# Optimization experiments

Hardware: AMD Instinct MI355X
Metric: run time of the kernel (lower is better)

The kernel has to match this reference:

```python
import jax, jax.numpy as jnp
import numpy as np

B, T, C, H = 4, 2048, 1024, 16
D = C // H  # head_dim = 64


def setup_inputs() -> dict:
    key = jax.random.key(0)
    k1, k2, k3 = jax.random.split(key, 3)
    x = jax.random.normal(k1, (B, T, C), dtype=jnp.float32)
    # nn.Linear weights: [out_features, in_features]
    W_attn = jax.random.normal(k2, (3 * C, C), dtype=jnp.float32) * (1.0 / np.sqrt(C))
    W_proj = jax.random.normal(k3, (C, C), dtype=jnp.float32) * (1.0 / np.sqrt(C))
    b_proj = jnp.zeros((C,), dtype=jnp.float32)
    return {"x": x, "W_attn": W_attn, "W_proj": W_proj, "b_proj": b_proj}


def reference(x, W_attn, W_proj, b_proj):
    Bx, Tx, Cx = x.shape
    # fused QKV projection (no bias), then split
    qkv = jnp.einsum('btc,oc->bto', x, W_attn)            # [B,T,3C]
    q, k, v = jnp.split(qkv, 3, axis=-1)                  # each [B,T,C]
    # [B,T,C] -> [B,H,T,D]
    def heads(t):
        return t.reshape(Bx, Tx, H, D).transpose(0, 2, 1, 3)
    q, k, v = heads(q), heads(k), heads(v)
    scale = 1.0 / np.sqrt(D).astype(np.float32)
    att = jnp.einsum('bhqd,bhkd->bhqk', q, k) * scale     # [B,H,T,T], no causal mask
    att = jax.nn.softmax(att, axis=-1)
    y = jnp.einsum('bhqk,bhkd->bhqd', att, v)             # [B,H,T,D]
    y = y.transpose(0, 2, 1, 3).reshape(Bx, Tx, Cx)       # [B,T,C]
    out = jnp.einsum('btc,oc->bto', y, W_proj) + b_proj   # output projection
    return out
```

## Files before the change

kernel.cpp:

```cpp
#include <hip/hip_runtime.h>


typedef _Float16 f16x8 __attribute__((ext_vector_type(8)));
typedef _Float16 f16x4 __attribute__((ext_vector_type(4)));
typedef _Float16 f16x2 __attribute__((ext_vector_type(2)));
typedef float f32x4 __attribute__((ext_vector_type(4)));

__device__ __forceinline__ void gl_lds16(const _Float16* g, _Float16* l) {
  __builtin_amdgcn_global_load_lds(
      (const __attribute__((address_space(1))) void*)g,
      (__attribute__((address_space(3))) void*)l, 16, 0, 0);
}

__device__ __forceinline__ float fexp2(float x) {
#if __has_builtin(__builtin_amdgcn_exp2f)
  return __builtin_amdgcn_exp2f(x);
#else
  return exp2f(x);
#endif
}

__global__ __launch_bounds__(256) void cvt_f32_f16(const float* __restrict__ src,
                                                   _Float16* __restrict__ dst, int n) {
  int i = (blockIdx.x * 256 + threadIdx.x) * 8;
  int stride = gridDim.x * 256 * 8;
  for (; i < n; i += stride) {
    float4 a = *(const float4*)(src + i);
    float4 b = *(const float4*)(src + i + 4);
    f16x8 o = {(_Float16)a.x, (_Float16)a.y, (_Float16)a.z, (_Float16)a.w,
               (_Float16)b.x, (_Float16)b.y, (_Float16)b.z, (_Float16)b.w};
    *(f16x8*)(dst + i) = o;
  }
}

template <bool BIAS, bool OUT_F16>
__global__ __launch_bounds__(256)
void gemm_bt(const _Float16* __restrict__ A, const _Float16* __restrict__ B,
             void* __restrict__ C, const float* __restrict__ bias,
             int M, int N, int K) {
  __shared__ _Float16 sA[128 * 64];
  __shared__ _Float16 sB[128 * 64];
  const int tid = threadIdx.x;
  const int w = tid >> 6, l = tid & 63, l15 = l & 15, l4 = l >> 4;
  const int wm = w >> 1, wn = w & 1;
  const size_t m0 = (size_t)blockIdx.y * 128, n0 = (size_t)blockIdx.x * 128;

  f32x4 acc[4][4] = {};

  const int sr = tid >> 3;
  const int sc8 = (tid & 7) ^ ((tid >> 3) & 7);
  const _Float16* aSrc = A + (m0 + sr) * (size_t)K + sc8 * 8;
  const _Float16* bSrc = B + (n0 + sr) * (size_t)K + sc8 * 8;
  _Float16* aDst = sA + tid * 8;
  _Float16* bDst = sB + tid * 8;
  const size_t K32 = 32 * (size_t)K;

  const int e7 = l15 & 7;

  for (int k0 = 0; k0 < K; k0 += 64) {
    __syncthreads();
#pragma unroll
    for (int j = 0; j < 4; ++j) {
      gl_lds16(aSrc + j * K32 + k0, aDst + j * 2048);
      gl_lds16(bSrc + j * K32 + k0, bDst + j * 2048);
    }
    __syncthreads();
#pragma unroll
    for (int ks = 0; ks < 2; ++ks) {
      const int cs_ = ((ks * 4 + l4) ^ e7) * 8;
      f16x8 af[4], bf[4];
#pragma unroll
      for (int i = 0; i < 4; ++i) {
        af[i] = *(const f16x8*)(sA + (wm * 64 + i * 16 + l15) * 64 + cs_);
        bf[i] = *(const f16x8*)(sB + (wn * 64 + i * 16 + l15) * 64 + cs_);
      }
#pragma unroll
      for (int i = 0; i < 4; ++i)
#pragma unroll
        for (int j = 0; j < 4; ++j)
          acc[i][j] = __builtin_amdgcn_mfma_f32_16x16x32_f16(af[i], bf[j], acc[i][j], 0, 0, 0);
    }
  }

#pragma unroll
  for (int i = 0; i < 4; ++i)
#pragma unroll
    for (int j = 0; j < 4; ++j) {
      size_t row = m0 + wm * 64 + i * 16 + l4 * 4;
      size_t col = n0 + wn * 64 + j * 16 + l15;
      float bv = 0.0f;
      if (BIAS) bv = bias[col];
#pragma unroll
      for (int rr = 0; rr < 4; ++rr) {
        float v = acc[i][j][rr] + bv;
        if (OUT_F16)
          ((_Float16*)C)[(row + rr) * N + col] = (_Float16)v;
        else
          ((float*)C)[(row + rr) * N + col] = v;
      }
    }
}

__global__ __launch_bounds__(256, 4)
void attn_kernel(const _Float16* __restrict__ qkv, _Float16* __restrict__ y16) {
  const int lin = blockIdx.x;
  const int xcd = lin & 7;
  const int bh = xcd * 8 + (lin >> 7);
  const int qt = (lin >> 3) & 15;
  const int b = bh >> 4, h = bh & 15;
  const int tid = threadIdx.x;
  const int w = tid >> 6, l = tid & 63, l15 = l & 15, l4 = l >> 4;

  __shared__ _Float16 sK[128 * 64];
  __shared__ _Float16 sVt[64][136];

  const size_t rowbase = (size_t)b * 2048;
  const int qcol = h * 64, kcol = 1024 + h * 64, vcol = 2048 + h * 64;

  f16x8 bq[2][2];
  {
    const _Float16 csf = (_Float16)(0.125f * 1.44269504f);
#pragma unroll
    for (int qs = 0; qs < 2; ++qs) {
      size_t qrow = rowbase + qt * 128 + w * 32 + qs * 16 + l15;
#pragma unroll
      for (int ks = 0; ks < 2; ++ks) {
        f16x8 v = *(const f16x8*)(qkv + qrow * 3072 + qcol + ks * 32 + l4 * 8);
#pragma unroll
        for (int e = 0; e < 8; ++e) v[e] *= csf;
        bq[qs][ks] = v;
      }
    }
  }

  f32x4 accy[2][4] = {};
  f32x4 accl[2] = {};

  const _Float16 one0 = (l15 == 0) ? (_Float16)1.0f : (_Float16)0.0f;
  const f16x4 bv1 = {one0, one0, one0, one0};

  const int krow = w * 8 + (l >> 3);
  const int csrc = (l & 7) ^ (l >> 3);
  const _Float16* kSrc0 = qkv + (rowbase + krow) * 3072 + kcol + csrc * 8;
  _Float16* kDst0 = sK + w * 8 * 64 + l * 8;

  const int vrow = 2 * l, vd0 = w * 16;
  const _Float16* vSrc0 = qkv + (rowbase + vrow) * 3072 + vcol + vd0;

  f16x8 va0 = *(const f16x8*)(vSrc0);
  f16x8 va1 = *(const f16x8*)(vSrc0 + 8);
  f16x8 vb0 = *(const f16x8*)(vSrc0 + 3072);
  f16x8 vb1 = *(const f16x8*)(vSrc0 + 3072 + 8);

  for (int kb = 0; kb < 16; ++kb) {
    __syncthreads();
    {
      const _Float16* ks_ = kSrc0 + (size_t)kb * 128 * 3072;
#pragma unroll
      for (int j = 0; j < 4; ++j) gl_lds16(ks_ + (size_t)j * 32 * 3072, kDst0 + j * 2048);
#pragma unroll
      for (int e = 0; e < 8; ++e) {
        f16x2 p0; p0[0] = va0[e]; p0[1] = vb0[e];
        *(f16x2*)(&sVt[vd0 + e][vrow]) = p0;
        f16x2 p1; p1[0] = va1[e]; p1[1] = vb1[e];
        *(f16x2*)(&sVt[vd0 + 8 + e][vrow]) = p1;
      }
    }
    __syncthreads();

    if (kb + 1 < 16) {
      const _Float16* vs_ = vSrc0 + (size_t)(kb + 1) * 128 * 3072;
      va0 = *(const f16x8*)(vs_);
      va1 = *(const f16x8*)(vs_ + 8);
      vb0 = *(const f16x8*)(vs_ + 3072);
      vb1 = *(const f16x8*)(vs_ + 3072 + 8);
    }

#pragma unroll
    for (int sub = 0; sub < 2; ++sub) {
      f32x4 st[2][4] = {};
      __builtin_amdgcn_s_setprio(1);
#pragma unroll
      for (int m = 0; m < 4; ++m) {
        const int row = sub * 64 + m * 16 + l15;
#pragma unroll
        for (int ks = 0; ks < 2; ++ks) {
          const int cs_ = (ks * 4 + l4) ^ (l15 & 7);
          f16x8 ak = *(const f16x8*)(sK + row * 64 + cs_ * 8);
          st[0][m] = __builtin_amdgcn_mfma_f32_16x16x32_f16(ak, bq[0][ks], st[0][m], 0, 0, 0);
          st[1][m] = __builtin_amdgcn_mfma_f32_16x16x32_f16(ak, bq[1][ks], st[1][m], 0, 0, 0);
        }
      }
      __builtin_amdgcn_s_setprio(0);

      f16x4 pa[2][4];
#pragma unroll
      for (int qs = 0; qs < 2; ++qs) {
#pragma unroll
        for (int m = 0; m < 4; ++m) {
          float p0 = fexp2(st[qs][m][0]);
          float p1 = fexp2(st[qs][m][1]);
          float p2 = fexp2(st[qs][m][2]);
          float p3 = fexp2(st[qs][m][3]);
#if __has_builtin(__builtin_amdgcn_cvt_pkrtz)
          auto lo = __builtin_amdgcn_cvt_pkrtz(p0, p1);
          auto hi = __builtin_amdgcn_cvt_pkrtz(p2, p3);
          f16x4 pv;
          pv[0] = lo[0]; pv[1] = lo[1]; pv[2] = hi[0]; pv[3] = hi[1];
          pa[qs][m] = pv;
#else
          f16x4 pv;
          pv[0] = (_Float16)p0; pv[1] = (_Float16)p1;
          pv[2] = (_Float16)p2; pv[3] = (_Float16)p3;
          pa[qs][m] = pv;
#endif
        }
      }

      __builtin_amdgcn_s_setprio(1);
#pragma unroll
      for (int m = 0; m < 4; ++m) {
        const int kc = sub * 64 + m * 16 + l4 * 4;
        accl[0] = __builtin_amdgcn_mfma_f32_16x16x16f16(bv1, pa[0][m], accl[0], 0, 0, 0);
        accl[1] = __builtin_amdgcn_mfma_f32_16x16x16f16(bv1, pa[1][m], accl[1], 0, 0, 0);
#pragma unroll
        for (int dt = 0; dt < 4; ++dt) {
          f16x4 bv = *(const f16x4*)(&sVt[dt * 16 + l15][kc]);
          accy[0][dt] = __builtin_amdgcn_mfma_f32_16x16x16f16(bv, pa[0][m], accy[0][dt], 0, 0, 0);
          accy[1][dt] = __builtin_amdgcn_mfma_f32_16x16x16f16(bv, pa[1][m], accy[1][dt], 0, 0, 0);
        }
      }
      __builtin_amdgcn_s_setprio(0);
    }
  }

#pragma unroll
  for (int qs = 0; qs < 2; ++qs) {
    const float lsum = __shfl(accl[qs][0], l15);
    const float rinv = 1.0f / lsum;
    const size_t row = rowbase + qt * 128 + w * 32 + qs * 16 + l15;
#pragma unroll
    for (int dt = 0; dt < 4; ++dt) {
      f16x4 ov;
#pragma unroll
      for (int r = 0; r < 4; ++r) ov[r] = (_Float16)(accy[qs][dt][r] * rinv);
      *(f16x4*)(y16 + row * 1024 + h * 64 + dt * 16 + l4 * 4) = ov;
    }
  }
}

extern "C" void kernel_launch(void* const* d_in, const int* in_sizes, int n_in,
                              void* d_out, int out_size, void* d_ws, size_t ws_size,
                              hipStream_t stream) {
  (void)in_sizes; (void)n_in; (void)out_size; (void)ws_size;
  const float* x  = (const float*)d_in[0];
  const float* Wa = (const float*)d_in[1];
  const float* Wp = (const float*)d_in[2];
  const float* bp = (const float*)d_in[3];
  float* out = (float*)d_out;

  char* ws = (char*)d_ws;
  _Float16* x16   = (_Float16*)ws; ws += (size_t)8192 * 1024 * 2;
  _Float16* Wa16  = (_Float16*)ws; ws += (size_t)3072 * 1024 * 2;
  _Float16* Wp16  = (_Float16*)ws; ws += (size_t)1024 * 1024 * 2;
  _Float16* qkv16 = (_Float16*)ws; ws += (size_t)8192 * 3072 * 2;
  _Float16* y16   = (_Float16*)ws; ws += (size_t)8192 * 1024 * 2;

  cvt_f32_f16<<<4096, 256, 0, stream>>>(x, x16, 8192 * 1024);
  cvt_f32_f16<<<1536, 256, 0, stream>>>(Wa, Wa16, 3072 * 1024);
  cvt_f32_f16<<<512, 256, 0, stream>>>(Wp, Wp16, 1024 * 1024);

  gemm_bt<false, true><<<dim3(24, 64), 256, 0, stream>>>(x16, Wa16, (void*)qkv16, nullptr,
                                                         8192, 3072, 1024);
  attn_kernel<<<1024, 256, 0, stream>>>(qkv16, y16);
  gemm_bt<true, false><<<dim3(8, 64), 256, 0, stream>>>(y16, Wp16, (void*)out, bp,
                                                        8192, 1024, 1024);
}
```

Measured before the change: 285.7 us.

## Use 16x16x32 MFMA for PV product via permuted K row loading

Switches the P·V and row-sum MFMAs from 16x16x16 to 16x16x32 instructions, concatenating two score tiles into an 8-wide f16 operand. For the K dimension of the 32-wide MFMA to line up with the S tile layout, K rows are loaded into shared memory in a permuted order (pkey), so score columns match V rows. This halves the number of PV MFMA issues and widens the LDS reads of V, at the cost of a subtle index permutation that must stay consistent.

```diff
diff --git a/kernel.cpp b/kernel.cpp
--- a/kernel.cpp
+++ b/kernel.cpp
@@ -137,11 +137,12 @@
   f32x4 accl[2] = {};
 
   const _Float16 one0 = (l15 == 0) ? (_Float16)1.0f : (_Float16)0.0f;
-  const f16x4 bv1 = {one0, one0, one0, one0};
-
-  const int krow = w * 8 + (l >> 3);
+  const f16x8 ones8 = {one0, one0, one0, one0, one0, one0, one0, one0};
+
+  const int rho = w * 8 + (l >> 3);
+  const int pkey = (rho & 3) | ((rho & 0x10) >> 2) | ((rho & 0xC) << 1);
   const int csrc = (l & 7) ^ (l >> 3);
-  const _Float16* kSrc0 = qkv + (rowbase + krow) * 3072 + kcol + csrc * 8;
+  const _Float16* kSrc0 = qkv + (rowbase + pkey) * 3072 + kcol + csrc * 8;
   _Float16* kDst0 = sK + w * 8 * 64 + l * 8;
 
   const int vrow = 2 * l, vd0 = w * 16;
@@ -193,41 +194,47 @@
       }
       __builtin_amdgcn_s_setprio(0);
 
-      f16x4 pa[2][4];
+      f16x8 pa8[2][2];
 #pragma unroll
       for (int qs = 0; qs < 2; ++qs) {
 #pragma unroll
-        for (int m = 0; m < 4; ++m) {
-          float p0 = fexp2(st[qs][m][0]);
-          float p1 = fexp2(st[qs][m][1]);
-          float p2 = fexp2(st[qs][m][2]);
-          float p3 = fexp2(st[qs][m][3]);
+        for (int c = 0; c < 2; ++c) {
+          f16x4 half_[2];
+#pragma unroll
+          for (int mm = 0; mm < 2; ++mm) {
+            const int m = 2 * c + mm;
+            float p0 = fexp2(st[qs][m][0]);
+            float p1 = fexp2(st[qs][m][1]);
+            float p2 = fexp2(st[qs][m][2]);
+            float p3 = fexp2(st[qs][m][3]);
 #if __has_builtin(__builtin_amdgcn_cvt_pkrtz)
-          auto lo = __builtin_amdgcn_cvt_pkrtz(p0, p1);
-          auto hi = __builtin_amdgcn_cvt_pkrtz(p2, p3);
-          f16x4 pv;
-          pv[0] = lo[0]; pv[1] = lo[1]; pv[2] = hi[0]; pv[3] = hi[1];
-          pa[qs][m] = pv;
+            auto lo = __builtin_amdgcn_cvt_pkrtz(p0, p1);
+            auto hi = __builtin_amdgcn_cvt_pkrtz(p2, p3);
+            f16x4 pv;
+            pv[0] = lo[0]; pv[1] = lo[1]; pv[2] = hi[0]; pv[3] = hi[1];
+            half_[mm] = pv;
 #else
-          f16x4 pv;
-          pv[0] = (_Float16)p0; pv[1] = (_Float16)p1;
-          pv[2] = (_Float16)p2; pv[3] = (_Float16)p3;
-          pa[qs][m] = pv;
+            f16x4 pv;
+            pv[0] = (_Float16)p0; pv[1] = (_Float16)p1;
+            pv[2] = (_Float16)p2; pv[3] = (_Float16)p3;
+            half_[mm] = pv;
 #endif
+          }
+          pa8[qs][c] = __builtin_shufflevector(half_[0], half_[1], 0, 1, 2, 3, 4, 5, 6, 7);
         }
       }
 
       __builtin_amdgcn_s_setprio(1);
 #pragma unroll
-      for (int m = 0; m < 4; ++m) {
-        const int kc = sub * 64 + m * 16 + l4 * 4;
-        accl[0] = __builtin_amdgcn_mfma_f32_16x16x16f16(bv1, pa[0][m], accl[0], 0, 0, 0);
-        accl[1] = __builtin_amdgcn_mfma_f32_16x16x16f16(bv1, pa[1][m], accl[1], 0, 0, 0);
+      for (int c = 0; c < 2; ++c) {
+        const int kc = sub * 64 + c * 32 + l4 * 8;
+        accl[0] = __builtin_amdgcn_mfma_f32_16x16x32_f16(ones8, pa8[0][c], accl[0], 0, 0, 0);
+        accl[1] = __builtin_amdgcn_mfma_f32_16x16x32_f16(ones8, pa8[1][c], accl[1], 0, 0, 0);
 #pragma unroll
         for (int dt = 0; dt < 4; ++dt) {
-          f16x4 bv = *(const f16x4*)(&sVt[dt * 16 + l15][kc]);
-          accy[0][dt] = __builtin_amdgcn_mfma_f32_16x16x16f16(bv, pa[0][m], accy[0][dt], 0, 0, 0);
-          accy[1][dt] = __builtin_amdgcn_mfma_f32_16x16x16f16(bv, pa[1][m], accy[1][dt], 0, 0, 0);
+          f16x8 av = *(const f16x8*)(&sVt[dt * 16 + l15][kc]);
+          accy[0][dt] = __builtin_amdgcn_mfma_f32_16x16x32_f16(av, pa8[0][c], accy[0][dt], 0, 0, 0);
+          accy[1][dt] = __builtin_amdgcn_mfma_f32_16x16x32_f16(av, pa8[1][c], accy[1][dt], 0, 0, 0);
         }
       }
       __builtin_amdgcn_s_setprio(0);
```

Result: faster. 269.9 us (-5.5%).
